# Performance work log

Hardware: AMD Instinct MI355X
Metric: run time of the kernel (lower is better)

Reference implementation:

```python
import jax, jax.numpy as jnp
import numpy as np

B, C, H, W = 2, 192, 256, 256
HEADS = 6


def _conv1x1(x, w, b):
    # x: [b,ci,h,w], w: [co,ci,1,1], b: [co]
    return jnp.einsum('oi,bihw->bohw', w[:, :, 0, 0], x) + b[None, :, None, None]


def _dwconv3x3(x, w, b):
    # depthwise 3x3, padding=1; x: [b,c,h,w], w: [c,1,3,3], b: [c]
    y = jax.lax.conv_general_dilated(
        x, w, window_strides=(1, 1), padding='SAME',
        feature_group_count=x.shape[1],
        dimension_numbers=('NCHW', 'OIHW', 'NCHW'))
    return y + b[None, :, None, None]


def _l2norm(t, eps=1e-12):
    # F.normalize(dim=-1): x / max(||x||_2, eps)
    n = jnp.sqrt(jnp.sum(t * t, axis=-1, keepdims=True))
    return t / jnp.maximum(n, eps)


def setup_inputs() -> dict:
    key = jax.random.key(0)
    ks = jax.random.split(key, 12)
    s = 0.02
    return {
        'feat_guide': jax.random.normal(ks[0], (B, C, H, W), jnp.float32),
        'feat_op': jax.random.normal(ks[1], (B, C, H, W), jnp.float32),
        'q_w': jax.random.normal(ks[2], (C, C, 1, 1), jnp.float32) * s,
        'q_b': jax.random.normal(ks[3], (C,), jnp.float32) * s,
        'kv_w': jax.random.normal(ks[4], (2 * C, C, 1, 1), jnp.float32) * s,
        'kv_b': jax.random.normal(ks[5], (2 * C,), jnp.float32) * s,
        'q_dw_w': jax.random.normal(ks[6], (C, 1, 3, 3), jnp.float32) * s,
        'q_dw_b': jax.random.normal(ks[7], (C,), jnp.float32) * s,
        'kv_dw_w': jax.random.normal(ks[8], (2 * C, 1, 3, 3), jnp.float32) * s,
        'kv_dw_b': jax.random.normal(ks[9], (2 * C,), jnp.float32) * s,
        'proj_w': jax.random.normal(ks[10], (C, C, 1, 1), jnp.float32) * s,
        'proj_b': jax.random.normal(ks[11], (C,), jnp.float32) * s,
        'temperature': jnp.ones((HEADS, 1, 1), jnp.float32),
    }


def reference(feat_guide, feat_op, q_w, q_b, kv_w, kv_b, q_dw_w, q_dw_b,
              kv_dw_w, kv_dw_b, proj_w, proj_b, temperature):
    b, c, h, w = feat_guide.shape
    q = _dwconv3x3(_conv1x1(feat_guide, q_w, q_b), q_dw_w, q_dw_b)
    kv = _dwconv3x3(_conv1x1(feat_op, kv_w, kv_b), kv_dw_w, kv_dw_b)
    k, v = jnp.split(kv, 2, axis=1)

    def heads(t):  # [b,c,h,w] -> [b,heads,c/heads,hw]
        return t.reshape(b, HEADS, c // HEADS, h * w)

    q = _l2norm(heads(q))
    k = _l2norm(heads(k))
    v = heads(v)
    # channel-wise attention: [b,heads,c',c'] scores over hw
    attn = jnp.einsum('bhcn,bhdn->bhcd', q, k) * temperature[None]
    attn = jax.nn.softmax(attn, axis=-1)
    out = jnp.einsum('bhcd,bhdn->bhcn', attn, v).reshape(b, c, h, w)
    return _conv1x1(out, proj_w, proj_b)
```

## Files before the change

### kernel.cpp

```cpp
#include <hip/hip_runtime.h>

#define HW_N 65536
#define CC 192
#define NCHUNKS 256

typedef __attribute__((ext_vector_type(8))) short short8v;
typedef __attribute__((ext_vector_type(4))) short short4v;
typedef __attribute__((ext_vector_type(4))) float f32x4;
typedef __attribute__((ext_vector_type(4))) int int4v;

__device__ __forceinline__ float bf2f(unsigned short u) {
  union { unsigned int i; float f; } v; v.i = ((unsigned int)u) << 16; return v.f;
}
__device__ __forceinline__ unsigned short f2bf(float f) {
  union { float f; unsigned int i; } v; v.f = f;
  unsigned int r = v.i + 0x7fffu + ((v.i >> 16) & 1u);
  return (unsigned short)(r >> 16);
}

__global__ __launch_bounds__(256) void cvt_w(
    const float* __restrict__ qw, const float* __restrict__ kvw,
    unsigned short* __restrict__ Wq, unsigned short* __restrict__ Wkv) {
  const int i = (blockIdx.x * 256 + threadIdx.x) * 8;
  const float* src; unsigned short* dst; int off;
  if (i < 36864) { src = qw; dst = Wq; off = i; }
  else { src = kvw; dst = Wkv; off = i - 36864; }
  unsigned short tmp[8];
#pragma unroll
  for (int j = 0; j < 8; ++j) tmp[j] = f2bf(src[off + j]);
  *(short8v*)(dst + off) = *(short8v*)tmp;
}

template <int INF32, int OUTF32>
__device__ __forceinline__ void gemm_body(
    const void* __restrict__ X_, const unsigned short* __restrict__ W,
    const float* __restrict__ bias, void* __restrict__ out_,
    int Mtot, int m0, int n0, int b, int t, unsigned char* smem) {
  typedef unsigned short row200[200];
  typedef unsigned short row152[152];
  row200* Bt = (row200*)smem;
  row152* Rp = (row152*)smem;
  const int lane = t & 63, wv = t >> 6;
  const int l15 = lane & 15, lg = lane >> 4;
  const int wm = wv & 3, wn = wv >> 2;
  const int mrow = m0 + wm * 48;
  const int nw = wn * 64;
  const size_t xbase = (size_t)b * CC * (size_t)HW_N + n0;

  for (int task = t; task < 768; task += 512) {
    const int kp = task >> 5, nq = task & 31;
    unsigned int p[8][2];
    if (INF32) {
      const float* Xf = (const float*)X_;
#pragma unroll
      for (int j = 0; j < 8; ++j) {
        f32x4 v = *(const f32x4*)(Xf + xbase + (size_t)(kp * 8 + j) * HW_N + nq * 4);
        p[j][0] = (unsigned int)f2bf(v[0]) | ((unsigned int)f2bf(v[1]) << 16);
        p[j][1] = (unsigned int)f2bf(v[2]) | ((unsigned int)f2bf(v[3]) << 16);
      }
    } else {
      const unsigned short* Xh = (const unsigned short*)X_;
#pragma unroll
      for (int j = 0; j < 8; ++j) {
        short4v v = *(const short4v*)(Xh + xbase + (size_t)(kp * 8 + j) * HW_N + nq * 4);
        p[j][0] = (unsigned int)(unsigned short)v[0] | ((unsigned int)(unsigned short)v[1] << 16);
        p[j][1] = (unsigned int)(unsigned short)v[2] | ((unsigned int)(unsigned short)v[3] << 16);
      }
    }
    const int kpx = kp ^ (nq & 7);
#pragma unroll
    for (int nn = 0; nn < 4; ++nn) {
      unsigned int q4[4];
#pragma unroll
      for (int wi = 0; wi < 4; ++wi) {
        const unsigned int lo = (p[2 * wi][nn >> 1] >> ((nn & 1) * 16)) & 0xffffu;
        const unsigned int hi = (p[2 * wi + 1][nn >> 1] >> ((nn & 1) * 16)) & 0xffffu;
        q4[wi] = lo | (hi << 16);
      }
      *(int4v*)&Bt[nq * 4 + nn][kpx * 8] = *(int4v*)q4;
    }
  }
  __syncthreads();

  f32x4 acc[3][4] = {};
#pragma unroll
  for (int kc = 0; kc < 6; ++kc) {
    const int k0 = kc * 32 + lg * 8;
    short8v af[3], bfr[4];
#pragma unroll
    for (int fr = 0; fr < 3; ++fr)
      af[fr] = *(const short8v*)(W + (size_t)(mrow + fr * 16 + l15) * CC + k0);
#pragma unroll
    for (int fc = 0; fc < 4; ++fc) {
      const int row = nw + fc * 16 + l15;
      const int oct = (kc * 4 + lg) ^ ((row >> 2) & 7);
      bfr[fc] = *(const short8v*)&Bt[row][oct * 8];
    }
#pragma unroll
    for (int fr = 0; fr < 3; ++fr)
#pragma unroll
      for (int fc = 0; fc < 4; ++fc)
        acc[fr][fc] = __builtin_amdgcn_mfma_f32_16x16x32_bf16(af[fr], bfr[fc], acc[fr][fc], 0, 0, 0);
  }

  const size_t obase = (size_t)b * Mtot * (size_t)HW_N;
  if (OUTF32) {
    float* outf = (float*)out_;
#pragma unroll
    for (int fr = 0; fr < 3; ++fr) {
      const int rbase = mrow + fr * 16 + lg * 4;
#pragma unroll
      for (int r = 0; r < 4; ++r) {
        const float bb = bias[rbase + r];
        const size_t ro = obase + (size_t)(rbase + r) * HW_N + n0 + nw;
#pragma unroll
        for (int fc = 0; fc < 4; ++fc)
          outf[ro + fc * 16 + l15] = acc[fr][fc][r] + bb;
      }
    }
    return;
  }
  __syncthreads();

#pragma unroll
  for (int half = 0; half < 2; ++half) {
    if ((wm >> 1) == half) {
      const int mbase = (wm & 1) * 48;
#pragma unroll
      for (int fr = 0; fr < 3; ++fr) {
#pragma unroll
        for (int r = 0; r < 4; ++r) {
          const int mloc = mbase + fr * 16 + lg * 4 + r;
          const float bb = bias[m0 + half * 96 + mloc];
#pragma unroll
          for (int fc = 0; fc < 4; ++fc)
            Rp[mloc][nw + fc * 16 + l15] = f2bf(acc[fr][fc][r] + bb);
        }
      }
    }
    __syncthreads();
#pragma unroll
    for (int s = 0; s < 3; ++s) {
      const int idx = s * 512 + t;
      const int m = idx >> 4, n8 = (idx & 15) * 8;
      short8v v = *(short8v*)&Rp[m][n8];
      const size_t oo = obase + (size_t)(m0 + half * 96 + m) * HW_N + n0 + n8;
      *(short8v*)((unsigned short*)out_ + oo) = v;
    }
    if (half == 0) __syncthreads();
  }
}

__global__ __launch_bounds__(512) void conv_gemm_qkv(
    const float* __restrict__ fg, const float* __restrict__ fo,
    const unsigned short* __restrict__ Wq, const unsigned short* __restrict__ Wkv,
    const float* __restrict__ q_b, const float* __restrict__ kv_b,
    unsigned short* __restrict__ QC, unsigned short* __restrict__ KVC) {
  __shared__ __align__(16) unsigned char smem[49152];
  typedef unsigned short row152[152];
  row152* Rp = (row152*)smem;
  const int d = blockIdx.x;
  const int b = blockIdx.z;
  const int t = threadIdx.x;
  const float* X; const unsigned short* W; const float* bias; unsigned short* out;
  int Mtot, m0, n0;
  if (d < 512) { X = fg; W = Wq; bias = q_b; out = QC; Mtot = 192; m0 = 0; n0 = d * 128; }
  else {
    const int dd = d - 512;
    const int mt = (dd >> 3) & 1;
    const int nt = (dd & 7) | ((dd >> 4) << 3);
    X = fo; W = Wkv; bias = kv_b; out = KVC; Mtot = 384; m0 = mt * 192; n0 = nt * 128;
  }
  const int lane = t & 63, wv = t >> 6;
  const int l15 = lane & 15, lg = lane >> 4;
  const int wm = wv & 3, wn = wv >> 2;
  const int mrow = m0 + wm * 48;
  const int nw = wn * 64;
  const size_t xbase = (size_t)b * CC * (size_t)HW_N + n0;

  auto issue = [&](int kc) {
    const int bsel = kc % 3;
#pragma unroll
    for (int i = 0; i < 2; ++i) {
      const int blk = wv * 2 + i;
      const int kl = blk * 2 + (lane >> 5);
      const int g = (lane & 31) ^ (((kl >> 3) & 1) << 2);
      const float* gp = X + xbase + (size_t)(kc * 32 + kl) * HW_N + g * 4;
      __builtin_amdgcn_global_load_lds(
          (const __attribute__((address_space(1))) void*)gp,
          (__attribute__((address_space(3))) void*)(smem + bsel * 16384 + blk * 1024),
          16, 0, 0);
    }
  };

  issue(0);
  issue(1);
  issue(2);

  f32x4 acc[3][4] = {};
#pragma unroll
  for (int kc = 0; kc < 6; ++kc) {
    if (kc < 4)      asm volatile("s_waitcnt vmcnt(4)" ::: "memory");
    else if (kc == 4) asm volatile("s_waitcnt vmcnt(2)" ::: "memory");
    else              asm volatile("s_waitcnt vmcnt(0)" ::: "memory");
    __builtin_amdgcn_s_barrier();

    const float* buf = (const float*)(smem + (kc % 3) * 16384);
    short8v af[3], bfr[4];
    const int k0 = kc * 32 + lg * 8;
#pragma unroll
    for (int fr = 0; fr < 3; ++fr)
      af[fr] = *(const short8v*)(W + (size_t)(mrow + fr * 16 + l15) * CC + k0);
#pragma unroll
    for (int fc = 0; fc < 4; ++fc) {
      const int nn = nw + fc * 16 + l15;
      const int sg = (((nn >> 2) ^ ((lg & 1) << 2)) << 2) + (nn & 3);
      unsigned short u[8];
#pragma unroll
      for (int j = 0; j < 8; ++j)
        u[j] = f2bf(buf[(lg * 8 + j) * 128 + sg]);
      bfr[fc] = *(short8v*)u;
    }
    asm volatile("s_waitcnt lgkmcnt(0)" ::: "memory");
    __builtin_amdgcn_sched_barrier(0);
    __builtin_amdgcn_s_barrier();
    if (kc < 3) issue(kc + 3);
#pragma unroll
    for (int fr = 0; fr < 3; ++fr)
#pragma unroll
      for (int fc = 0; fc < 4; ++fc)
        acc[fr][fc] = __builtin_amdgcn_mfma_f32_16x16x32_bf16(af[fr], bfr[fc], acc[fr][fc], 0, 0, 0);
  }

  const size_t obase = (size_t)b * Mtot * (size_t)HW_N;
  __syncthreads();
#pragma unroll
  for (int half = 0; half < 2; ++half) {
    if ((wm >> 1) == half) {
      const int mbase = (wm & 1) * 48;
#pragma unroll
      for (int fr = 0; fr < 3; ++fr) {
#pragma unroll
        for (int r = 0; r < 4; ++r) {
          const int mloc = mbase + fr * 16 + lg * 4 + r;
          const float bb = bias[m0 + half * 96 + mloc];
#pragma unroll
          for (int fc = 0; fc < 4; ++fc)
            Rp[mloc][nw + fc * 16 + l15] = f2bf(acc[fr][fc][r] + bb);
        }
      }
    }
    __syncthreads();
#pragma unroll
    for (int s = 0; s < 3; ++s) {
      const int idx = s * 512 + t;
      const int m = idx >> 4, n8 = (idx & 15) * 8;
      short8v v = *(short8v*)&Rp[m][n8];
      const size_t oo = obase + (size_t)(m0 + half * 96 + m) * HW_N + n0 + n8;
      *(short8v*)(out + oo) = v;
    }
    if (half == 0) __syncthreads();
  }
}

__global__ __launch_bounds__(512) void conv_gemm_final(
    const unsigned short* __restrict__ Vb, const unsigned short* __restrict__ Mw,
    const float* __restrict__ proj_b, float* __restrict__ out) {
  __shared__ __align__(16) unsigned char smem[51200];
  const int b = blockIdx.z;
  gemm_body<0, 1>((const void*)Vb, Mw + (size_t)b * CC * CC, proj_b, (void*)out,
                  192, 0, blockIdx.x * 128, b, threadIdx.x, smem);
}

__global__ __launch_bounds__(256) void dwconv3x3_all(
    const unsigned short* __restrict__ QC, const unsigned short* __restrict__ KVC,
    const float* __restrict__ q_dw_w, const float* __restrict__ q_dw_b,
    const float* __restrict__ kv_dw_w, const float* __restrict__ kv_dw_b,
    unsigned short* __restrict__ Qb, unsigned short* __restrict__ Kb,
    unsigned short* __restrict__ Vb) {
  const int t = threadIdx.x;
  const int wc = (t & 31) * 8;
  const int h0 = blockIdx.x * 32 + (t >> 5) * 4;
  const int y = blockIdx.y, b = blockIdx.z;
  const unsigned short* in; const float* w; float bv; unsigned short* out;
  if (y < 192) {
    in = QC + ((size_t)b * 192 + y) * (size_t)HW_N;
    w = q_dw_w + y * 9; bv = q_dw_b[y];
    out = Qb + ((size_t)b * 192 + y) * (size_t)HW_N;
  } else if (y < 384) {
    const int c = y - 192;
    in = KVC + ((size_t)b * 384 + c) * (size_t)HW_N;
    w = kv_dw_w + c * 9; bv = kv_dw_b[c];
    out = Kb + ((size_t)b * 192 + c) * (size_t)HW_N;
  } else {
    const int c = y - 384;
    in = KVC + ((size_t)b * 384 + 192 + c) * (size_t)HW_N;
    w = kv_dw_w + (192 + c) * 9; bv = kv_dw_b[192 + c];
    out = Vb + ((size_t)b * 192 + c) * (size_t)HW_N;
  }
  float wv9[9];
#pragma unroll
  for (int i = 0; i < 9; ++i) wv9[i] = w[i];
  float f[6][10];
#pragma unroll
  for (int ky = 0; ky < 6; ++ky) {
    const int hh = h0 + ky - 1;
    if (hh < 0 || hh > 255) {
#pragma unroll
      for (int j = 0; j < 10; ++j) f[ky][j] = 0.f;
    } else {
      const unsigned short* row = in + hh * 256;
      short8v v = *(const short8v*)(row + wc);
      f[ky][0] = (wc > 0) ? bf2f(row[wc - 1]) : 0.f;
#pragma unroll
      for (int j = 0; j < 8; ++j) f[ky][1 + j] = bf2f((unsigned short)v[j]);
      f[ky][9] = (wc < 248) ? bf2f(row[wc + 8]) : 0.f;
    }
  }
#pragma unroll
  for (int rr = 0; rr < 4; ++rr) {
    union { short8v v; unsigned short u[8]; } o;
#pragma unroll
    for (int j = 0; j < 8; ++j) {
      float acc = bv;
#pragma unroll
      for (int ky = 0; ky < 3; ++ky)
#pragma unroll
        for (int kx = 0; kx < 3; ++kx)
          acc += wv9[ky * 3 + kx] * f[rr + ky][j + kx];
      o.u[j] = f2bf(acc);
    }
    *(short8v*)(out + (h0 + rr) * 256 + wc) = o.v;
  }
}

__global__ __launch_bounds__(64) void gram_kernel(
    const unsigned short* __restrict__ Q, const unsigned short* __restrict__ K,
    float* __restrict__ Gp, float* __restrict__ nqp, float* __restrict__ nkp) {
  const int lane = threadIdx.x;
  const int l15 = lane & 15, lg = lane >> 4;
  const int chunk = blockIdx.x, h = blockIdx.y, b = blockIdx.z;
  const int bh = b * 6 + h;
  const size_t base = ((size_t)b * CC + h * 32) * (size_t)HW_N;
  f32x4 acc[2][2] = {};
  float sq[2] = {0.f, 0.f}, sk[2] = {0.f, 0.f};
  const int nst = chunk * 256 + lg * 8;
  for (int ks = 0; ks < 8; ++ks) {
    const int n = nst + ks * 32;
    short8v qa[2], kb[2];
#pragma unroll
    for (int fr = 0; fr < 2; ++fr) {
      qa[fr] = *(const short8v*)(Q + base + (size_t)(fr * 16 + l15) * HW_N + n);
      kb[fr] = *(const short8v*)(K + base + (size_t)(fr * 16 + l15) * HW_N + n);
    }
#pragma unroll
    for (int fr = 0; fr < 2; ++fr)
#pragma unroll
      for (int j = 0; j < 8; ++j) {
        float a = bf2f((unsigned short)qa[fr][j]); sq[fr] += a * a;
        float c2 = bf2f((unsigned short)kb[fr][j]); sk[fr] += c2 * c2;
      }
#pragma unroll
    for (int fr = 0; fr < 2; ++fr)
#pragma unroll
      for (int fc = 0; fc < 2; ++fc)
        acc[fr][fc] = __builtin_amdgcn_mfma_f32_16x16x32_bf16(qa[fr], kb[fc], acc[fr][fc], 0, 0, 0);
  }
  float* Gb = Gp + (size_t)(chunk * 12 + bh) * 1024;
#pragma unroll
  for (int fr = 0; fr < 2; ++fr)
#pragma unroll
    for (int fc = 0; fc < 2; ++fc)
#pragma unroll
      for (int r = 0; r < 4; ++r)
        Gb[(fr * 16 + lg * 4 + r) * 32 + fc * 16 + l15] = acc[fr][fc][r];
#pragma unroll
  for (int fr = 0; fr < 2; ++fr) {
    float v = sq[fr]; v += __shfl_down(v, 32); v += __shfl_down(v, 16);
    float u = sk[fr]; u += __shfl_down(u, 32); u += __shfl_down(u, 16);
    if (lane < 16) {
      nqp[(size_t)(chunk * 12 + bh) * 32 + fr * 16 + lane] = v;
      nkp[(size_t)(chunk * 12 + bh) * 32 + fr * 16 + lane] = u;
    }
  }
}

__global__ __launch_bounds__(256) void attn_proj_fused(
    const float* __restrict__ Gp, const float* __restrict__ nqp, const float* __restrict__ nkp,
    const float* __restrict__ temp, const float* __restrict__ proj_w,
    unsigned short* __restrict__ Mout) {
  const int h = blockIdx.x, b = blockIdx.y;
  const int bh = b * 6 + h;
  const int t = threadIdx.x;
  __shared__ float sc[32][33];
  __shared__ float nrmq[32], nrmk[32];

  f32x4 gs = {0.f, 0.f, 0.f, 0.f};
  const float* gbase = Gp + (size_t)bh * 1024 + t * 4;
  for (int ch = 0; ch < NCHUNKS; ++ch) {
    f32x4 v = *(const f32x4*)(gbase + (size_t)ch * 12288);
    gs[0] += v[0]; gs[1] += v[1]; gs[2] += v[2]; gs[3] += v[3];
  }
  {
    const int c = t >> 3, d0 = (t * 4) & 31;
#pragma unroll
    for (int j = 0; j < 4; ++j) sc[c][d0 + j] = gs[j];
  }
  if (t < 64) {
    const float* np = (t < 32 ? nqp : nkp) + (size_t)bh * 32 + (t & 31);
    float s = 0.f;
    for (int ch = 0; ch < NCHUNKS; ++ch) s += np[(size_t)ch * 384];
    if (t < 32) nrmq[t] = fmaxf(sqrtf(s), 1e-12f);
    else nrmk[t - 32] = fmaxf(sqrtf(s), 1e-12f);
  }
  __syncthreads();
  const float tpr = temp[h];
  for (int i = t; i < 1024; i += 256) {
    const int c = i >> 5, d = i & 31;
    sc[c][d] = sc[c][d] * tpr / (nrmq[c] * nrmk[d]);
  }
  __syncthreads();
  if (t < 32) {
    float mx = -1e30f;
    for (int d = 0; d < 32; ++d) mx = fmaxf(mx, sc[t][d]);
    float sum = 0.f;
    for (int d = 0; d < 32; ++d) { float e = __expf(sc[t][d] - mx); sc[t][d] = e; sum += e; }
    const float inv = 1.f / sum;
    for (int d = 0; d < 32; ++d) sc[t][d] *= inv;
  }
  __syncthreads();
  for (int i = t; i < 6144; i += 256) {
    const int co = i >> 5, d = i & 31;
    float acc = 0.f;
    for (int c = 0; c < 32; ++c) acc += proj_w[co * CC + h * 32 + c] * sc[c][d];
    Mout[((size_t)b * CC + co) * CC + h * 32 + d] = f2bf(acc);
  }
}

extern "C" void kernel_launch(void* const* d_in, const int* in_sizes, int n_in,
                              void* d_out, int out_size, void* d_ws, size_t ws_size,
                              hipStream_t stream) {
  const float* fg = (const float*)d_in[0];
  const float* fo = (const float*)d_in[1];
  const float* q_w = (const float*)d_in[2];
  const float* q_b = (const float*)d_in[3];
  const float* kv_w = (const float*)d_in[4];
  const float* kv_b = (const float*)d_in[5];
  const float* q_dw_w = (const float*)d_in[6];
  const float* q_dw_b = (const float*)d_in[7];
  const float* kv_dw_w = (const float*)d_in[8];
  const float* kv_dw_b = (const float*)d_in[9];
  const float* proj_w = (const float*)d_in[10];
  const float* proj_b = (const float*)d_in[11];
  const float* temp = (const float*)d_in[12];

  char* ws = (char*)d_ws;
  unsigned short* QC  = (unsigned short*)(ws + 0);
  unsigned short* KVC = (unsigned short*)(ws + 50331648);
  unsigned short* Qb  = (unsigned short*)(ws + 150994944);
  unsigned short* Kb  = (unsigned short*)(ws + 0);
  unsigned short* Vb  = (unsigned short*)(ws + 50331648);
  float* Gp  = (float*)(ws + 100663296);
  float* nqp = (float*)(ws + 113246208);
  float* nkp = (float*)(ws + 113639424);
  unsigned short* Mw  = (unsigned short*)(ws + 208063488);
  unsigned short* Wq  = (unsigned short*)(ws + 208210944);
  unsigned short* Wkv = (unsigned short*)(ws + 208284672);

  cvt_w<<<dim3(54), dim3(256), 0, stream>>>(q_w, kv_w, Wq, Wkv);
  conv_gemm_qkv<<<dim3(1536, 1, 2), dim3(512), 0, stream>>>(
      fg, fo, Wq, Wkv, q_b, kv_b, QC, KVC);
  dwconv3x3_all<<<dim3(8, 576, 2), dim3(256), 0, stream>>>(
      QC, KVC, q_dw_w, q_dw_b, kv_dw_w, kv_dw_b, Qb, Kb, Vb);
  gram_kernel<<<dim3(NCHUNKS, 6, 2), dim3(64), 0, stream>>>(Qb, Kb, Gp, nqp, nkp);
  attn_proj_fused<<<dim3(6, 2), dim3(256), 0, stream>>>(
      Gp, nqp, nkp, temp, proj_w, Mw);
  conv_gemm_final<<<dim3(512, 1, 2), dim3(512), 0, stream>>>(Vb, Mw, proj_b, (float*)d_out);
}
```

Baseline: 266.3 us.

## Fuse V depthwise conv into final projection GEMM prologue

Removes the V branch from the standalone depthwise-conv kernel and instead computes the 3x3 depthwise conv for V on the fly while staging the B tile of the final projection GEMM. This avoids writing and re-reading the intermediate V buffer in global memory. In exchange, each GEMM block reads three input rows per channel plus halo elements and does extra ALU work before the MFMA loop, and workspace offsets are moved so the gram partials no longer alias the KV buffer that must now stay live.

```diff
diff --git a/kernel.cpp b/kernel.cpp
--- a/kernel.cpp
+++ b/kernel.cpp
@@ -29,126 +29,6 @@
 #pragma unroll
   for (int j = 0; j < 8; ++j) tmp[j] = f2bf(src[off + j]);
   *(short8v*)(dst + off) = *(short8v*)tmp;
-}
-
-template <int INF32, int OUTF32>
-__device__ __forceinline__ void gemm_body(
-    const void* __restrict__ X_, const unsigned short* __restrict__ W,
-    const float* __restrict__ bias, void* __restrict__ out_,
-    int Mtot, int m0, int n0, int b, int t, unsigned char* smem) {
-  typedef unsigned short row200[200];
-  typedef unsigned short row152[152];
-  row200* Bt = (row200*)smem;
-  row152* Rp = (row152*)smem;
-  const int lane = t & 63, wv = t >> 6;
-  const int l15 = lane & 15, lg = lane >> 4;
-  const int wm = wv & 3, wn = wv >> 2;
-  const int mrow = m0 + wm * 48;
-  const int nw = wn * 64;
-  const size_t xbase = (size_t)b * CC * (size_t)HW_N + n0;
-
-  for (int task = t; task < 768; task += 512) {
-    const int kp = task >> 5, nq = task & 31;
-    unsigned int p[8][2];
-    if (INF32) {
-      const float* Xf = (const float*)X_;
-#pragma unroll
-      for (int j = 0; j < 8; ++j) {
-        f32x4 v = *(const f32x4*)(Xf + xbase + (size_t)(kp * 8 + j) * HW_N + nq * 4);
-        p[j][0] = (unsigned int)f2bf(v[0]) | ((unsigned int)f2bf(v[1]) << 16);
-        p[j][1] = (unsigned int)f2bf(v[2]) | ((unsigned int)f2bf(v[3]) << 16);
-      }
-    } else {
-      const unsigned short* Xh = (const unsigned short*)X_;
-#pragma unroll
-      for (int j = 0; j < 8; ++j) {
-        short4v v = *(const short4v*)(Xh + xbase + (size_t)(kp * 8 + j) * HW_N + nq * 4);
-        p[j][0] = (unsigned int)(unsigned short)v[0] | ((unsigned int)(unsigned short)v[1] << 16);
-        p[j][1] = (unsigned int)(unsigned short)v[2] | ((unsigned int)(unsigned short)v[3] << 16);
-      }
-    }
-    const int kpx = kp ^ (nq & 7);
-#pragma unroll
-    for (int nn = 0; nn < 4; ++nn) {
-      unsigned int q4[4];
-#pragma unroll
-      for (int wi = 0; wi < 4; ++wi) {
-        const unsigned int lo = (p[2 * wi][nn >> 1] >> ((nn & 1) * 16)) & 0xffffu;
-        const unsigned int hi = (p[2 * wi + 1][nn >> 1] >> ((nn & 1) * 16)) & 0xffffu;
-        q4[wi] = lo | (hi << 16);
-      }
-      *(int4v*)&Bt[nq * 4 + nn][kpx * 8] = *(int4v*)q4;
-    }
-  }
-  __syncthreads();
-
-  f32x4 acc[3][4] = {};
-#pragma unroll
-  for (int kc = 0; kc < 6; ++kc) {
-    const int k0 = kc * 32 + lg * 8;
-    short8v af[3], bfr[4];
-#pragma unroll
-    for (int fr = 0; fr < 3; ++fr)
-      af[fr] = *(const short8v*)(W + (size_t)(mrow + fr * 16 + l15) * CC + k0);
-#pragma unroll
-    for (int fc = 0; fc < 4; ++fc) {
-      const int row = nw + fc * 16 + l15;
-      const int oct = (kc * 4 + lg) ^ ((row >> 2) & 7);
-      bfr[fc] = *(const short8v*)&Bt[row][oct * 8];
-    }
-#pragma unroll
-    for (int fr = 0; fr < 3; ++fr)
-#pragma unroll
-      for (int fc = 0; fc < 4; ++fc)
-        acc[fr][fc] = __builtin_amdgcn_mfma_f32_16x16x32_bf16(af[fr], bfr[fc], acc[fr][fc], 0, 0, 0);
-  }
-
-  const size_t obase = (size_t)b * Mtot * (size_t)HW_N;
-  if (OUTF32) {
-    float* outf = (float*)out_;
-#pragma unroll
-    for (int fr = 0; fr < 3; ++fr) {
-      const int rbase = mrow + fr * 16 + lg * 4;
-#pragma unroll
-      for (int r = 0; r < 4; ++r) {
-        const float bb = bias[rbase + r];
-        const size_t ro = obase + (size_t)(rbase + r) * HW_N + n0 + nw;
-#pragma unroll
-        for (int fc = 0; fc < 4; ++fc)
-          outf[ro + fc * 16 + l15] = acc[fr][fc][r] + bb;
-      }
-    }
-    return;
-  }
-  __syncthreads();
-
-#pragma unroll
-  for (int half = 0; half < 2; ++half) {
-    if ((wm >> 1) == half) {
-      const int mbase = (wm & 1) * 48;
-#pragma unroll
-      for (int fr = 0; fr < 3; ++fr) {
-#pragma unroll
-        for (int r = 0; r < 4; ++r) {
-          const int mloc = mbase + fr * 16 + lg * 4 + r;
-          const float bb = bias[m0 + half * 96 + mloc];
-#pragma unroll
-          for (int fc = 0; fc < 4; ++fc)
-            Rp[mloc][nw + fc * 16 + l15] = f2bf(acc[fr][fc][r] + bb);
-        }
-      }
-    }
-    __syncthreads();
-#pragma unroll
-    for (int s = 0; s < 3; ++s) {
-      const int idx = s * 512 + t;
-      const int m = idx >> 4, n8 = (idx & 15) * 8;
-      short8v v = *(short8v*)&Rp[m][n8];
-      const size_t oo = obase + (size_t)(m0 + half * 96 + m) * HW_N + n0 + n8;
-      *(short8v*)((unsigned short*)out_ + oo) = v;
-    }
-    if (half == 0) __syncthreads();
-  }
 }
 
 __global__ __launch_bounds__(512) void conv_gemm_qkv(
@@ -200,7 +80,7 @@
   f32x4 acc[3][4] = {};
 #pragma unroll
   for (int kc = 0; kc < 6; ++kc) {
-    if (kc < 4)      asm volatile("s_waitcnt vmcnt(4)" ::: "memory");
+    if (kc < 4)       asm volatile("s_waitcnt vmcnt(4)" ::: "memory");
     else if (kc == 4) asm volatile("s_waitcnt vmcnt(2)" ::: "memory");
     else              asm volatile("s_waitcnt vmcnt(0)" ::: "memory");
     __builtin_amdgcn_s_barrier();
@@ -263,21 +143,119 @@
   }
 }
 
-__global__ __launch_bounds__(512) void conv_gemm_final(
-    const unsigned short* __restrict__ Vb, const unsigned short* __restrict__ Mw,
+__global__ __launch_bounds__(512) void conv_gemm_final_dwv(
+    const unsigned short* __restrict__ KVC, const float* __restrict__ kv_dw_w,
+    const float* __restrict__ kv_dw_b, const unsigned short* __restrict__ Mw,
     const float* __restrict__ proj_b, float* __restrict__ out) {
   __shared__ __align__(16) unsigned char smem[51200];
+  typedef unsigned short row200[200];
+  row200* Bt = (row200*)smem;
+  const int d = blockIdx.x;
   const int b = blockIdx.z;
-  gemm_body<0, 1>((const void*)Vb, Mw + (size_t)b * CC * CC, proj_b, (void*)out,
-                  192, 0, blockIdx.x * 128, b, threadIdx.x, smem);
+  const int t = threadIdx.x;
+  const int h = d >> 1;
+  const int col0 = (d & 1) * 128;
+  const int n0 = d * 128;
+  const unsigned short* W = Mw + (size_t)b * CC * CC;
+  const int lane = t & 63, wv = t >> 6;
+  const int l15 = lane & 15, lg = lane >> 4;
+  const int wm = wv & 3, wn = wv >> 2;
+  const int mrow = wm * 48;
+  const int nw = wn * 64;
+
+  for (int task = t; task < 768; task += 512) {
+    const int kp4 = task >> 4;
+    const int g = task & 15;
+    const int w0 = col0 + g * 8;
+    unsigned short res[4][8];
+#pragma unroll
+    for (int cj = 0; cj < 4; ++cj) {
+      const int ch = kp4 * 4 + cj;
+      const unsigned short* src = KVC + ((size_t)b * 384 + 192 + ch) * (size_t)HW_N;
+      const float* wp = kv_dw_w + (192 + ch) * 9;
+      float wv9[9];
+#pragma unroll
+      for (int i = 0; i < 9; ++i) wv9[i] = wp[i];
+      const float bv = kv_dw_b[192 + ch];
+      float f[3][10];
+#pragma unroll
+      for (int ky = 0; ky < 3; ++ky) {
+        const int r2 = h + ky - 1;
+        if (r2 < 0 || r2 > 255) {
+#pragma unroll
+          for (int j = 0; j < 10; ++j) f[ky][j] = 0.f;
+        } else {
+          const unsigned short* rp = src + r2 * 256;
+          short8v v = *(const short8v*)(rp + w0);
+          f[ky][0] = (w0 > 0) ? bf2f(rp[w0 - 1]) : 0.f;
+#pragma unroll
+          for (int j = 0; j < 8; ++j) f[ky][1 + j] = bf2f((unsigned short)v[j]);
+          f[ky][9] = (w0 < 248) ? bf2f(rp[w0 + 8]) : 0.f;
+        }
+      }
+#pragma unroll
+      for (int px = 0; px < 8; ++px) {
+        float a = bv;
+#pragma unroll
+        for (int ky = 0; ky < 3; ++ky)
+#pragma unroll
+          for (int kx = 0; kx < 3; ++kx)
+            a += wv9[ky * 3 + kx] * f[ky][px + kx];
+        res[cj][px] = f2bf(a);
+      }
+    }
+    const int kp = kp4 >> 1, hoff = (kp4 & 1) * 4;
+#pragma unroll
+    for (int r = 0; r < 8; ++r) {
+      const int row = g * 8 + r;
+      const int kpx = kp ^ ((row >> 2) & 7);
+      unsigned short pk4[4] = {res[0][r], res[1][r], res[2][r], res[3][r]};
+      *(short4v*)&Bt[row][kpx * 8 + hoff] = *(short4v*)pk4;
+    }
+  }
+  __syncthreads();
+
+  f32x4 acc[3][4] = {};
+#pragma unroll
+  for (int kc = 0; kc < 6; ++kc) {
+    const int k0 = kc * 32 + lg * 8;
+    short8v af[3], bfr[4];
+#pragma unroll
+    for (int fr = 0; fr < 3; ++fr)
+      af[fr] = *(const short8v*)(W + (size_t)(mrow + fr * 16 + l15) * CC + k0);
+#pragma unroll
+    for (int fc = 0; fc < 4; ++fc) {
+      const int row = nw + fc * 16 + l15;
+      const int oct = (kc * 4 + lg) ^ ((row >> 2) & 7);
+      bfr[fc] = *(const short8v*)&Bt[row][oct * 8];
+    }
+#pragma unroll
+    for (int fr = 0; fr < 3; ++fr)
+#pragma unroll
+      for (int fc = 0; fc < 4; ++fc)
+        acc[fr][fc] = __builtin_amdgcn_mfma_f32_16x16x32_bf16(af[fr], bfr[fc], acc[fr][fc], 0, 0, 0);
+  }
+
+  const size_t obase = (size_t)b * CC * (size_t)HW_N;
+#pragma unroll
+  for (int fr = 0; fr < 3; ++fr) {
+    const int rbase = mrow + fr * 16 + lg * 4;
+#pragma unroll
+    for (int r = 0; r < 4; ++r) {
+      const float bb = proj_b[rbase + r];
+      const size_t ro = obase + (size_t)(rbase + r) * HW_N + n0 + nw;
+#pragma unroll
+      for (int fc = 0; fc < 4; ++fc)
+        out[ro + fc * 16 + l15] = acc[fr][fc][r] + bb;
+    }
+  }
 }
 
 __global__ __launch_bounds__(256) void dwconv3x3_all(
     const unsigned short* __restrict__ QC, const unsigned short* __restrict__ KVC,
     const float* __restrict__ q_dw_w, const float* __restrict__ q_dw_b,
     const float* __restrict__ kv_dw_w, const float* __restrict__ kv_dw_b,
-    unsigned short* __restrict__ Qb, unsigned short* __restrict__ Kb,
-    unsigned short* __restrict__ Vb) {
+    unsigned short* __restrict__ Qb, unsigned short* __restrict__ Kb) {
   const int t = threadIdx.x;
   const int wc = (t & 31) * 8;
   const int h0 = blockIdx.x * 32 + (t >> 5) * 4;
@@ -287,16 +265,11 @@
     in = QC + ((size_t)b * 192 + y) * (size_t)HW_N;
     w = q_dw_w + y * 9; bv = q_dw_b[y];
     out = Qb + ((size_t)b * 192 + y) * (size_t)HW_N;
-  } else if (y < 384) {
+  } else {
     const int c = y - 192;
     in = KVC + ((size_t)b * 384 + c) * (size_t)HW_N;
     w = kv_dw_w + c * 9; bv = kv_dw_b[c];
     out = Kb + ((size_t)b * 192 + c) * (size_t)HW_N;
-  } else {
-    const int c = y - 384;
-    in = KVC + ((size_t)b * 384 + 192 + c) * (size_t)HW_N;
-    w = kv_dw_w + (192 + c) * 9; bv = kv_dw_b[192 + c];
-    out = Vb + ((size_t)b * 192 + c) * (size_t)HW_N;
   }
   float wv9[9];
 #pragma unroll
@@ -459,10 +432,9 @@
   unsigned short* KVC = (unsigned short*)(ws + 50331648);
   unsigned short* Qb  = (unsigned short*)(ws + 150994944);
   unsigned short* Kb  = (unsigned short*)(ws + 0);
-  unsigned short* Vb  = (unsigned short*)(ws + 50331648);
-  float* Gp  = (float*)(ws + 100663296);
-  float* nqp = (float*)(ws + 113246208);
-  float* nkp = (float*)(ws + 113639424);
+  float* Gp  = (float*)(ws + 209715200);
+  float* nqp = (float*)(ws + 222298112);
+  float* nkp = (float*)(ws + 222691328);
   unsigned short* Mw  = (unsigned short*)(ws + 208063488);
   unsigned short* Wq  = (unsigned short*)(ws + 208210944);
   unsigned short* Wkv = (unsigned short*)(ws + 208284672);
@@ -470,10 +442,11 @@
   cvt_w<<<dim3(54), dim3(256), 0, stream>>>(q_w, kv_w, Wq, Wkv);
   conv_gemm_qkv<<<dim3(1536, 1, 2), dim3(512), 0, stream>>>(
       fg, fo, Wq, Wkv, q_b, kv_b, QC, KVC);
-  dwconv3x3_all<<<dim3(8, 576, 2), dim3(256), 0, stream>>>(
-      QC, KVC, q_dw_w, q_dw_b, kv_dw_w, kv_dw_b, Qb, Kb, Vb);
+  dwconv3x3_all<<<dim3(8, 384, 2), dim3(256), 0, stream>>>(
+      QC, KVC, q_dw_w, q_dw_b, kv_dw_w, kv_dw_b, Qb, Kb);
   gram_kernel<<<dim3(NCHUNKS, 6, 2), dim3(64), 0, stream>>>(Qb, Kb, Gp, nqp, nkp);
   attn_proj_fused<<<dim3(6, 2), dim3(256), 0, stream>>>(
       Gp, nqp, nkp, temp, proj_w, Mw);
-  conv_gemm_final<<<dim3(512, 1, 2), dim3(512), 0, stream>>>(Vb, Mw, proj_b, (float*)d_out);
-}
+  conv_gemm_final_dwv<<<dim3(512, 1, 2), dim3(512), 0, stream>>>(
+      KVC, kv_dw_w, kv_dw_b, Mw, proj_b, (float*)d_out);
+}
```

Measured after the change: 328.3 us. 23.3% more time.
